# Performance work log

Hardware: AMD Instinct MI355X
Metric: run time of the kernel (lower is better)

Reference implementation:

```python
import jax, jax.numpy as jnp
import numpy as np

B, S, DK = 32, 2048, 64

def setup_inputs() -> dict:
    key = jax.random.key(0)
    kq, kk, kv = jax.random.split(key, 3)
    Q = jax.random.normal(kq, (B, S, DK), dtype=jnp.float32)
    K = jax.random.normal(kk, (B, S, DK), dtype=jnp.float32)
    V = jax.random.normal(kv, (B, S, DK), dtype=jnp.float32)
    return {"Q": Q, "K": K, "V": V}

def reference(Q, K, V):
    # attn_scores = Q K^T / sqrt(d_k); full [B,S,S] probs materialized (naive, non-flash)
    d_k = Q.shape[-1]
    scores = jnp.einsum('bqd,bkd->bqk', Q, K) / jnp.sqrt(jnp.asarray(d_k, Q.dtype))
    probs = jax.nn.softmax(scores, axis=-1)
    return jnp.einsum('bqk,bkd->bqd', probs, V)
```

## Files before the change

### kernel.cpp

```cpp
#include <hip/hip_runtime.h>

#define BATCH 32
#define SEQ   2048
#define DKK   64

constexpr int QT = 128;
constexpr int KT = 64;
constexpr int NW = 8;
constexpr int WQ = 16;

typedef __attribute__((ext_vector_type(8))) short bf16x8;
typedef __attribute__((ext_vector_type(4))) float f32x4;
typedef __attribute__((ext_vector_type(4))) short short4v;

__device__ __forceinline__ short f2bf(float f) {
    union { float f; unsigned u; } c; c.f = f;
    unsigned r = c.u + 0x7fffu + ((c.u >> 16) & 1u);
    return (short)(r >> 16);
}

__device__ __forceinline__ unsigned pack2(short lo, short hi) {
    return (unsigned)(unsigned short)lo | ((unsigned)(unsigned short)hi << 16);
}

__device__ __forceinline__ float fast_exp2(float x) {
#if __has_builtin(__builtin_amdgcn_exp2f)
    return __builtin_amdgcn_exp2f(x);
#else
    return exp2f(x);
#endif
}

__global__ __launch_bounds__(512, 4) void attn_fwd(
        const float* __restrict__ Q, const float* __restrict__ K,
        const float* __restrict__ V, float* __restrict__ O) {
    __shared__ short Kb[KT][72];
    __shared__ short Vt[DKK][72];
    __shared__ short Pb[NW][WQ][72];

    const int tid  = threadIdx.x;
    const int w    = tid >> 6;
    const int lane = tid & 63;
    const int quad = lane >> 4;
    const int l15  = lane & 15;
    const int b    = blockIdx.y;
    const int q0   = blockIdx.x * QT + w * WQ;

    const float qscale = 0.125f * 1.44269504088896340736f;
    bf16x8 qfrag[2];
    #pragma unroll
    for (int ks = 0; ks < 2; ++ks) {
        const float* qp = Q + ((size_t)b * SEQ + q0 + l15) * DKK + 32*ks + quad*8;
        float4 a = *(const float4*)qp;
        float4 c = *(const float4*)(qp + 4);
        bf16x8 f;
        f[0]=f2bf(a.x*qscale); f[1]=f2bf(a.y*qscale); f[2]=f2bf(a.z*qscale); f[3]=f2bf(a.w*qscale);
        f[4]=f2bf(c.x*qscale); f[5]=f2bf(c.y*qscale); f[6]=f2bf(c.z*qscale); f[7]=f2bf(c.w*qscale);
        qfrag[ks] = f;
    }

    f32x4 o[4] = {};
    float lsum = 0.f;

    const float* Kbase = K + (size_t)b * SEQ * DKK;
    const float* Vbase = V + (size_t)b * SEQ * DKK;

    const int krow = tid >> 4;
    const int kcol = (tid & 15) << 2;
    const int kg   = (w & 3) * 16 + 4 * quad;
    const int d0   = l15 + 16 * (2 * (w >> 2));
    const int d1   = d0 + 16;

    float4 kpre0, kpre1;
    float  vpre0[4], vpre1[4];
    auto load_tile = [&](int kb) {
        const float* Kg = Kbase + (size_t)kb * DKK;
        kpre0 = *(const float4*)(Kg + krow * DKK + kcol);
        kpre1 = *(const float4*)(Kg + (krow + 32) * DKK + kcol);
        const float* Vp = Vbase + (size_t)(kb + kg) * DKK;
        #pragma unroll
        for (int i = 0; i < 4; ++i) vpre0[i] = Vp[i * DKK + d0];
        #pragma unroll
        for (int i = 0; i < 4; ++i) vpre1[i] = Vp[i * DKK + d1];
    };

    load_tile(0);

    for (int kb = 0; kb < SEQ; kb += KT) {
        __syncthreads();
        {
            short4v kk;
            kk[0]=f2bf(kpre0.x); kk[1]=f2bf(kpre0.y); kk[2]=f2bf(kpre0.z); kk[3]=f2bf(kpre0.w);
            *(short4v*)&Kb[krow][kcol] = kk;
            kk[0]=f2bf(kpre1.x); kk[1]=f2bf(kpre1.y); kk[2]=f2bf(kpre1.z); kk[3]=f2bf(kpre1.w);
            *(short4v*)&Kb[krow + 32][kcol] = kk;
            short4v t;
            t[0]=f2bf(vpre0[0]); t[1]=f2bf(vpre0[1]); t[2]=f2bf(vpre0[2]); t[3]=f2bf(vpre0[3]);
            *(short4v*)&Vt[d0][kg] = t;
            t[0]=f2bf(vpre1[0]); t[1]=f2bf(vpre1[1]); t[2]=f2bf(vpre1[2]); t[3]=f2bf(vpre1[3]);
            *(short4v*)&Vt[d1][kg] = t;
        }
        __syncthreads();

        load_tile((kb + KT) & (SEQ - 1));

        f32x4 sc[4];
        #pragma unroll
        for (int kt = 0; kt < 4; ++kt) {
            bf16x8 kf0 = *(const bf16x8*)&Kb[16*kt + l15][quad*8];
            bf16x8 kf1 = *(const bf16x8*)&Kb[16*kt + l15][32 + quad*8];
            f32x4 acc = {};
            acc = __builtin_amdgcn_mfma_f32_16x16x32_bf16(kf0, qfrag[0], acc, 0, 0, 0);
            acc = __builtin_amdgcn_mfma_f32_16x16x32_bf16(kf1, qfrag[1], acc, 0, 0, 0);
            sc[kt] = acc;
        }

        #pragma unroll
        for (int kt = 0; kt < 4; ++kt) {
            float p0 = fast_exp2(sc[kt][0]);
            float p1 = fast_exp2(sc[kt][1]);
            float p2 = fast_exp2(sc[kt][2]);
            float p3 = fast_exp2(sc[kt][3]);
            lsum += (p0 + p1) + (p2 + p3);
            int2 pw;
            pw.x = (int)pack2(f2bf(p0), f2bf(p1));
            pw.y = (int)pack2(f2bf(p2), f2bf(p3));
            *(int2*)&Pb[w][l15][16*kt + 4*quad] = pw;
        }

        #pragma unroll
        for (int ks = 0; ks < 2; ++ks) {
            bf16x8 pf = *(const bf16x8*)&Pb[w][l15][32*ks + quad*8];
            #pragma unroll
            for (int nt = 0; nt < 4; ++nt) {
                bf16x8 vf = *(const bf16x8*)&Vt[16*nt + l15][32*ks + quad*8];
                o[nt] = __builtin_amdgcn_mfma_f32_16x16x32_bf16(vf, pf, o[nt], 0, 0, 0);
            }
        }
    }

    float s = lsum;
    s += __shfl_xor(s, 16);
    s += __shfl_xor(s, 32);
    const float inv = 1.0f / s;

    float* op = O + ((size_t)b * SEQ + q0 + l15) * DKK + 4*quad;
    #pragma unroll
    for (int nt = 0; nt < 4; ++nt) {
        float4 st;
        st.x = o[nt][0] * inv;
        st.y = o[nt][1] * inv;
        st.z = o[nt][2] * inv;
        st.w = o[nt][3] * inv;
        *(float4*)(op + 16*nt) = st;
    }
}

extern "C" void kernel_launch(void* const* d_in, const int* in_sizes, int n_in,
                              void* d_out, int out_size, void* d_ws, size_t ws_size,
                              hipStream_t stream) {
    const float* Q = (const float*)d_in[0];
    const float* K = (const float*)d_in[1];
    const float* V = (const float*)d_in[2];
    float* O = (float*)d_out;
    dim3 grid(SEQ / QT, BATCH);
    attn_fwd<<<grid, dim3(512), 0, stream>>>(Q, K, V, O);
}
```

Measured before the change: 150.7 us.

## Double-buffer K/V tiles in LDS and use packed bf16 conversion intrinsic

```diff
diff --git a/kernel.cpp b/kernel.cpp
--- a/kernel.cpp
+++ b/kernel.cpp
@@ -1,26 +1,22 @@
 #include <hip/hip_runtime.h>
+#include <hip/hip_bf16.h>
 
 #define BATCH 32
 #define SEQ   2048
 #define DKK   64
 
-constexpr int QT = 128;
-constexpr int KT = 64;
-constexpr int NW = 8;
-constexpr int WQ = 16;
+constexpr int QT  = 128;
+constexpr int KT  = 64;
+constexpr int NW  = 8;
+constexpr int NIT = SEQ / KT;
 
 typedef __attribute__((ext_vector_type(8))) short bf16x8;
 typedef __attribute__((ext_vector_type(4))) float f32x4;
-typedef __attribute__((ext_vector_type(4))) short short4v;
 
-__device__ __forceinline__ short f2bf(float f) {
-    union { float f; unsigned u; } c; c.f = f;
-    unsigned r = c.u + 0x7fffu + ((c.u >> 16) & 1u);
-    return (short)(r >> 16);
-}
-
-__device__ __forceinline__ unsigned pack2(short lo, short hi) {
-    return (unsigned)(unsigned short)lo | ((unsigned)(unsigned short)hi << 16);
+__device__ __forceinline__ unsigned cvt2(float a, float b) {
+    union { __hip_bfloat162 h; unsigned u; } c;
+    c.h = __float22bfloat162_rn(make_float2(a, b));
+    return c.u;
 }
 
 __device__ __forceinline__ float fast_exp2(float x) {
@@ -34,9 +30,9 @@
 __global__ __launch_bounds__(512, 4) void attn_fwd(
         const float* __restrict__ Q, const float* __restrict__ K,
         const float* __restrict__ V, float* __restrict__ O) {
-    __shared__ short Kb[KT][72];
-    __shared__ short Vt[DKK][72];
-    __shared__ short Pb[NW][WQ][72];
+    __shared__ short Kb[2][KT][72];
+    __shared__ short Vt[2][DKK][72];
+    __shared__ short Pb[NW][16][72];
 
     const int tid  = threadIdx.x;
     const int w    = tid >> 6;
@@ -44,19 +40,21 @@
     const int quad = lane >> 4;
     const int l15  = lane & 15;
     const int b    = blockIdx.y;
-    const int q0   = blockIdx.x * QT + w * WQ;
+    const int q0   = blockIdx.x * QT + w * 16;
 
     const float qscale = 0.125f * 1.44269504088896340736f;
     bf16x8 qfrag[2];
     #pragma unroll
-    for (int ks = 0; ks < 2; ++ks) {
-        const float* qp = Q + ((size_t)b * SEQ + q0 + l15) * DKK + 32*ks + quad*8;
+    for (int h = 0; h < 2; ++h) {
+        const float* qp = Q + ((size_t)b * SEQ + q0 + l15) * DKK + 32*h + quad*8;
         float4 a = *(const float4*)qp;
         float4 c = *(const float4*)(qp + 4);
-        bf16x8 f;
-        f[0]=f2bf(a.x*qscale); f[1]=f2bf(a.y*qscale); f[2]=f2bf(a.z*qscale); f[3]=f2bf(a.w*qscale);
-        f[4]=f2bf(c.x*qscale); f[5]=f2bf(c.y*qscale); f[6]=f2bf(c.z*qscale); f[7]=f2bf(c.w*qscale);
-        qfrag[ks] = f;
+        union { bf16x8 v; unsigned u[4]; } f;
+        f.u[0] = cvt2(a.x*qscale, a.y*qscale);
+        f.u[1] = cvt2(a.z*qscale, a.w*qscale);
+        f.u[2] = cvt2(c.x*qscale, c.y*qscale);
+        f.u[3] = cvt2(c.z*qscale, c.w*qscale);
+        qfrag[h] = f.v;
     }
 
     f32x4 o[4] = {};
@@ -71,44 +69,44 @@
     const int d0   = l15 + 16 * (2 * (w >> 2));
     const int d1   = d0 + 16;
 
-    float4 kpre0, kpre1;
-    float  vpre0[4], vpre1[4];
-    auto load_tile = [&](int kb) {
-        const float* Kg = Kbase + (size_t)kb * DKK;
-        kpre0 = *(const float4*)(Kg + krow * DKK + kcol);
-        kpre1 = *(const float4*)(Kg + (krow + 32) * DKK + kcol);
-        const float* Vp = Vbase + (size_t)(kb + kg) * DKK;
+    float4 kp0, kp1;
+    float  vp0[4], vp1[4];
+    auto load_regs = [&](int t) {
+        const float* Kg = Kbase + (size_t)(t * KT) * DKK;
+        kp0 = *(const float4*)(Kg + krow * DKK + kcol);
+        kp1 = *(const float4*)(Kg + (krow + 32) * DKK + kcol);
+        const float* Vp = Vbase + (size_t)(t * KT + kg) * DKK;
         #pragma unroll
-        for (int i = 0; i < 4; ++i) vpre0[i] = Vp[i * DKK + d0];
+        for (int i = 0; i < 4; ++i) vp0[i] = Vp[i * DKK + d0];
         #pragma unroll
-        for (int i = 0; i < 4; ++i) vpre1[i] = Vp[i * DKK + d1];
+        for (int i = 0; i < 4; ++i) vp1[i] = Vp[i * DKK + d1];
+    };
+    auto write_lds = [&](int buf) {
+        int2 kk;
+        kk.x = (int)cvt2(kp0.x, kp0.y); kk.y = (int)cvt2(kp0.z, kp0.w);
+        *(int2*)&Kb[buf][krow][kcol] = kk;
+        kk.x = (int)cvt2(kp1.x, kp1.y); kk.y = (int)cvt2(kp1.z, kp1.w);
+        *(int2*)&Kb[buf][krow + 32][kcol] = kk;
+        int2 t;
+        t.x = (int)cvt2(vp0[0], vp0[1]); t.y = (int)cvt2(vp0[2], vp0[3]);
+        *(int2*)&Vt[buf][d0][kg] = t;
+        t.x = (int)cvt2(vp1[0], vp1[1]); t.y = (int)cvt2(vp1[2], vp1[3]);
+        *(int2*)&Vt[buf][d1][kg] = t;
     };
 
-    load_tile(0);
+    load_regs(0);
+    write_lds(0);
+    load_regs(1);
+    __syncthreads();
 
-    for (int kb = 0; kb < SEQ; kb += KT) {
-        __syncthreads();
-        {
-            short4v kk;
-            kk[0]=f2bf(kpre0.x); kk[1]=f2bf(kpre0.y); kk[2]=f2bf(kpre0.z); kk[3]=f2bf(kpre0.w);
-            *(short4v*)&Kb[krow][kcol] = kk;
-            kk[0]=f2bf(kpre1.x); kk[1]=f2bf(kpre1.y); kk[2]=f2bf(kpre1.z); kk[3]=f2bf(kpre1.w);
-            *(short4v*)&Kb[krow + 32][kcol] = kk;
-            short4v t;
-            t[0]=f2bf(vpre0[0]); t[1]=f2bf(vpre0[1]); t[2]=f2bf(vpre0[2]); t[3]=f2bf(vpre0[3]);
-            *(short4v*)&Vt[d0][kg] = t;
-            t[0]=f2bf(vpre1[0]); t[1]=f2bf(vpre1[1]); t[2]=f2bf(vpre1[2]); t[3]=f2bf(vpre1[3]);
-            *(short4v*)&Vt[d1][kg] = t;
-        }
-        __syncthreads();
-
-        load_tile((kb + KT) & (SEQ - 1));
+    for (int it = 0; it < NIT; ++it) {
+        const int cur = it & 1;
 
         f32x4 sc[4];
         #pragma unroll
         for (int kt = 0; kt < 4; ++kt) {
-            bf16x8 kf0 = *(const bf16x8*)&Kb[16*kt + l15][quad*8];
-            bf16x8 kf1 = *(const bf16x8*)&Kb[16*kt + l15][32 + quad*8];
+            bf16x8 kf0 = *(const bf16x8*)&Kb[cur][16*kt + l15][quad*8];
+            bf16x8 kf1 = *(const bf16x8*)&Kb[cur][16*kt + l15][32 + quad*8];
             f32x4 acc = {};
             acc = __builtin_amdgcn_mfma_f32_16x16x32_bf16(kf0, qfrag[0], acc, 0, 0, 0);
             acc = __builtin_amdgcn_mfma_f32_16x16x32_bf16(kf1, qfrag[1], acc, 0, 0, 0);
@@ -123,8 +121,8 @@
             float p3 = fast_exp2(sc[kt][3]);
             lsum += (p0 + p1) + (p2 + p3);
             int2 pw;
-            pw.x = (int)pack2(f2bf(p0), f2bf(p1));
-            pw.y = (int)pack2(f2bf(p2), f2bf(p3));
+            pw.x = (int)cvt2(p0, p1);
+            pw.y = (int)cvt2(p2, p3);
             *(int2*)&Pb[w][l15][16*kt + 4*quad] = pw;
         }
 
@@ -133,9 +131,15 @@
             bf16x8 pf = *(const bf16x8*)&Pb[w][l15][32*ks + quad*8];
             #pragma unroll
             for (int nt = 0; nt < 4; ++nt) {
-                bf16x8 vf = *(const bf16x8*)&Vt[16*nt + l15][32*ks + quad*8];
+                bf16x8 vf = *(const bf16x8*)&Vt[cur][16*nt + l15][32*ks + quad*8];
                 o[nt] = __builtin_amdgcn_mfma_f32_16x16x32_bf16(vf, pf, o[nt], 0, 0, 0);
             }
+        }
+
+        if (it + 1 < NIT) {
+            write_lds(1 - cur);
+            if (it + 2 < NIT) load_regs(it + 2);
+            __syncthreads();
         }
     }
 
```

After: 144.3 us. -4.2%, faster.
